# Kernel tuning notes

Measured on AMD Instinct MI355X. Metric: run time of the kernel, lower is better.

Reference implementation:

```python
import jax, jax.numpy as jnp
import numpy as np

NUM_USERS = 50000
EMBED_DIM = 128
NUM_EDGES = 800000


def setup_inputs() -> dict:
    key = jax.random.key(0)
    k1, k2, k3, k4, k5 = jax.random.split(key, 5)
    user_emb = jax.random.normal(k1, (NUM_USERS, EMBED_DIM), dtype=jnp.float32)
    # xavier_uniform init for the square weight
    limit = float(np.sqrt(6.0 / (EMBED_DIM + EMBED_DIM)))
    social_weight = jax.random.uniform(k2, (EMBED_DIM, EMBED_DIM), dtype=jnp.float32,
                                       minval=-limit, maxval=limit)
    rows = jax.random.randint(k3, (NUM_EDGES,), 0, NUM_USERS)  # destination nodes
    cols = jax.random.randint(k4, (NUM_EDGES,), 0, NUM_USERS)  # source nodes
    vals = jax.random.uniform(k5, (NUM_EDGES,), dtype=jnp.float32)  # adjacency weights
    return {"user_emb": user_emb, "social_weight": social_weight,
            "rows": rows, "cols": cols, "vals": vals}


def reference(user_emb, social_weight, rows, cols, vals):
    # weighted_emb = user_emb @ W  (dense GEMM)
    weighted = jnp.matmul(user_emb, social_weight)  # [N, D]
    # neighbor_emb = sparse.mm(adj, weighted): out[i] = sum_{e: rows[e]==i} vals[e] * weighted[cols[e]]
    gathered = weighted[cols] * vals[:, None]  # [E, D]
    neighbor = jax.ops.segment_sum(gathered, rows, num_segments=user_emb.shape[0])  # [N, D]
    # dropout is identity in eval mode; residual add
    return user_emb + neighbor
```

## Files before the change

### kernel.cpp

```cpp
#include <hip/hip_runtime.h>

#define DD 128
#define CAP 32
#define OVF_MAX 4096
#define EPB 2048
#define BSHIFT 10
#define NBKT_MAX 64
#define BCAP 24576

typedef __attribute__((ext_vector_type(8))) short short8;
typedef __attribute__((ext_vector_type(4))) float f32x4;

static __device__ __forceinline__ unsigned pack_bf16_2(float lo, float hi) {
  return __builtin_amdgcn_perm(__float_as_uint(hi) + 0x8000u,
                               __float_as_uint(lo) + 0x8000u, 0x07060302u);
}
static __device__ __forceinline__ unsigned short f2bf(float f) {
  return (unsigned short)((__float_as_uint(f) + 0x8000u) >> 16);
}
static __device__ __forceinline__ float bf2f(unsigned short h) {
  return __uint_as_float((unsigned)h << 16);
}

__global__ __launch_bounds__(256) void p1_bucket(
    const float* __restrict__ W, unsigned short* __restrict__ Wtg,
    const int* __restrict__ rows, const int* __restrict__ cols,
    const float* __restrict__ vals, int* __restrict__ binctr,
    int2* __restrict__ bucket, int* __restrict__ ovf_cnt,
    int4* __restrict__ ovf, int E, int nbkt) {
  const int t = threadIdx.x;
  if (blockIdx.x == 0) {
    const int k0 = (t >> 4) * 8;
    const int n0 = (t & 15) * 8;
    float v[8][8];
#pragma unroll
    for (int kk = 0; kk < 8; ++kk) {
      float4 a = *(const float4*)(W + (k0 + kk) * DD + n0);
      float4 b = *(const float4*)(W + (k0 + kk) * DD + n0 + 4);
      v[kk][0] = a.x; v[kk][1] = a.y; v[kk][2] = a.z; v[kk][3] = a.w;
      v[kk][4] = b.x; v[kk][5] = b.y; v[kk][6] = b.z; v[kk][7] = b.w;
    }
#pragma unroll
    for (int nn = 0; nn < 8; ++nn) {
      uint4 d;
      d.x = pack_bf16_2(v[0][nn], v[1][nn]);
      d.y = pack_bf16_2(v[2][nn], v[3][nn]);
      d.z = pack_bf16_2(v[4][nn], v[5][nn]);
      d.w = pack_bf16_2(v[6][nn], v[7][nn]);
      *(uint4*)(Wtg + (size_t)(n0 + nn) * DD + k0) = d;
    }
    return;
  }

  __shared__ int lrow[EPB];
  __shared__ int hist[NBKT_MAX];
  __shared__ int gbase[NBKT_MAX];
  __shared__ int lcur[NBKT_MAX];

  const int c0 = (blockIdx.x - 1) * EPB;
  const int n = min(EPB, E - c0);

  if (t < NBKT_MAX) { hist[t] = 0; lcur[t] = 0; }
  __syncthreads();

  for (int i = t; i < n; i += 256) {
    const int r = rows[c0 + i];
    lrow[i] = r;
    atomicAdd(&hist[r >> BSHIFT], 1);
  }
  __syncthreads();

  if (t < nbkt && hist[t] > 0) gbase[t] = atomicAdd(&binctr[t], hist[t]);
  __syncthreads();

  for (int i = t; i < n; i += 256) {
    const int r = lrow[i];
    const int b = r >> BSHIFT;
    const int lpos = atomicAdd(&lcur[b], 1);
    const int idx = gbase[b] + lpos;
    const int col = cols[c0 + i];
    const float v = vals[c0 + i];
    if (idx < BCAP) {
      bucket[(size_t)b * BCAP + idx] =
          make_int2(((r & 1023) << 22) | col, __float_as_int(v));
    } else {
      const int o = atomicAdd(ovf_cnt, 1);
      if (o < OVF_MAX) ovf[o] = make_int4(r, col, __float_as_int(v), 0);
    }
  }
}

#define WTS 136
__global__ __launch_bounds__(256) void p2k2_fused(
    const int* __restrict__ binctr, const int2* __restrict__ bucket,
    int* __restrict__ counts, int2* __restrict__ spair,
    int* __restrict__ ovf_cnt, int4* __restrict__ ovf,
    const float* __restrict__ U, const unsigned short* __restrict__ Wtg,
    unsigned short* __restrict__ wb, float* __restrict__ out, int N,
    int nbkt, int do_copy) {
  __shared__ union {
    unsigned short Wt[DD][WTS];
    int scnt[1 << BSHIFT];
  } sm;
  const int t = threadIdx.x;

  if ((int)blockIdx.x < nbkt) {
    const int b = blockIdx.x;
    const int base = b << BSHIFT;
    const int nrows = min(1 << BSHIFT, N - base);
    for (int i = t; i < (1 << BSHIFT); i += 256) sm.scnt[i] = 0;
    __syncthreads();

    const int nb = min(binctr[b], BCAP);
    const int2* __restrict__ bkt = bucket + (size_t)b * BCAP;
    for (int i = t; i < nb; i += 256) {
      const int2 p = bkt[i];
      const int lr = (unsigned)p.x >> 22;
      const int col = p.x & 0x3FFFFF;
      const int slot = atomicAdd(&sm.scnt[lr], 1);
      if (slot < CAP) {
        spair[(size_t)(base + lr) * CAP + slot] = make_int2(col, p.y);
      } else {
        const int o = atomicAdd(ovf_cnt, 1);
        if (o < OVF_MAX) ovf[o] = make_int4(base + lr, col, p.y, 0);
      }
    }
    __syncthreads();
    for (int i = t; i < nrows; i += 256) counts[base + i] = sm.scnt[i];
    return;
  }

  const int gb = blockIdx.x - nbkt;
#pragma unroll
  for (int i = 0; i < 8; ++i) {
    const int s = t + 256 * i;
    const int nn = s >> 4;
    const int k0 = (s & 15) * 8;
    uint4 d = *(const uint4*)(Wtg + (size_t)nn * DD + k0);
    *(uint4*)(&sm.Wt[nn][k0]) = d;
  }

  const int blk_row0 = gb * 128;
  if (do_copy) {
    const int nrow = min(128, N - blk_row0);
    const float4* U4 = (const float4*)(U + (size_t)blk_row0 * DD);
    float4* O4 = (float4*)(out + (size_t)blk_row0 * DD);
    for (int i = t; i < nrow * 32; i += 256) O4[i] = U4[i];
  }
  __syncthreads();

  const int w = t >> 6;
  const int lane = t & 63;
  const int m = lane & 15;
  const int quad = lane >> 4;
  const int row_base = blk_row0 + w * 32;

  short8 afrag[2][4];
#pragma unroll
  for (int s = 0; s < 2; ++s) {
    const int r = min(row_base + s * 16 + m, N - 1);
    const float* up = U + (size_t)r * DD + quad * 8;
#pragma unroll
    for (int c = 0; c < 4; ++c) {
      float4 x = *(const float4*)(up + c * 32);
      float4 y = *(const float4*)(up + c * 32 + 4);
      union { unsigned u[4]; short8 v; } fr;
      fr.u[0] = pack_bf16_2(x.x, x.y);
      fr.u[1] = pack_bf16_2(x.z, x.w);
      fr.u[2] = pack_bf16_2(y.x, y.y);
      fr.u[3] = pack_bf16_2(y.z, y.w);
      afrag[s][c] = fr.v;
    }
  }

  f32x4 acc[2][8];
#pragma unroll
  for (int s = 0; s < 2; ++s)
#pragma unroll
    for (int ct = 0; ct < 8; ++ct) acc[s][ct] = (f32x4){0.f, 0.f, 0.f, 0.f};

#pragma unroll
  for (int c = 0; c < 4; ++c) {
#pragma unroll
    for (int ct = 0; ct < 8; ++ct) {
      short8 bfrag = *(const short8*)&sm.Wt[ct * 16 + m][c * 32 + quad * 8];
      acc[0][ct] = __builtin_amdgcn_mfma_f32_16x16x32_bf16(
          afrag[0][c], bfrag, acc[0][ct], 0, 0, 0);
      acc[1][ct] = __builtin_amdgcn_mfma_f32_16x16x32_bf16(
          afrag[1][c], bfrag, acc[1][ct], 0, 0, 0);
    }
  }

#pragma unroll
  for (int s = 0; s < 2; ++s) {
    const int rb = row_base + s * 16 + quad * 4;
#pragma unroll
    for (int ct = 0; ct < 8; ++ct) {
#pragma unroll
      for (int reg = 0; reg < 4; ++reg) {
        const int r = rb + reg;
        if (r < N) wb[(size_t)r * DD + ct * 16 + m] = f2bf(acc[s][ct][reg]);
      }
    }
  }
}

__global__ __launch_bounds__(256) void k3_accumulate(
    const int* __restrict__ counts, const int2* __restrict__ spair,
    const unsigned short* __restrict__ wb, const float* __restrict__ U,
    const int* __restrict__ ovf_cnt, const int4* __restrict__ ovf,
    float* __restrict__ out, int N) {
  const int r = blockIdx.x * 4 + (threadIdx.x >> 6);
  if (r >= N) return;
  const int lane = threadIdx.x & 63;

  const ushort2* __restrict__ WB2 = (const ushort2*)wb;
  float2 acc = ((const float2*)U)[(size_t)r * 64 + lane];

  const int cnt = min(counts[r], CAP);
  const int2* __restrict__ lst = spair + (size_t)r * CAP;

  int i = 0;
  for (; i + 8 <= cnt; i += 8) {
    int2 p[8];
#pragma unroll
    for (int j = 0; j < 8; ++j) p[j] = lst[i + j];
    ushort2 a[8];
#pragma unroll
    for (int j = 0; j < 8; ++j) a[j] = WB2[(size_t)p[j].x * 64 + lane];
#pragma unroll
    for (int j = 0; j < 8; ++j) {
      const float v = __int_as_float(p[j].y);
      acc.x = fmaf(v, bf2f(a[j].x), acc.x);
      acc.y = fmaf(v, bf2f(a[j].y), acc.y);
    }
  }
  for (; i + 2 <= cnt; i += 2) {
    const int2 p0 = lst[i];
    const int2 p1 = lst[i + 1];
    const ushort2 a0 = WB2[(size_t)p0.x * 64 + lane];
    const ushort2 a1 = WB2[(size_t)p1.x * 64 + lane];
    const float v0 = __int_as_float(p0.y);
    const float v1 = __int_as_float(p1.y);
    acc.x = fmaf(v0, bf2f(a0.x), acc.x);
    acc.y = fmaf(v0, bf2f(a0.y), acc.y);
    acc.x = fmaf(v1, bf2f(a1.x), acc.x);
    acc.y = fmaf(v1, bf2f(a1.y), acc.y);
  }
  if (i < cnt) {
    const int2 p0 = lst[i];
    const ushort2 a0 = WB2[(size_t)p0.x * 64 + lane];
    const float v0 = __int_as_float(p0.y);
    acc.x = fmaf(v0, bf2f(a0.x), acc.x);
    acc.y = fmaf(v0, bf2f(a0.y), acc.y);
  }

  const int nov = min(*ovf_cnt, OVF_MAX);
  if (nov > 0) {
    for (int o = 0; o < nov; ++o) {
      const int4 e = ovf[o];
      if (e.x == r) {
        const float v = __int_as_float(e.z);
        const ushort2 a = WB2[(size_t)e.y * 64 + lane];
        acc.x = fmaf(v, bf2f(a.x), acc.x);
        acc.y = fmaf(v, bf2f(a.y), acc.y);
      }
    }
  }

  ((float2*)out)[(size_t)r * 64 + lane] = acc;
}

__global__ __launch_bounds__(256) void scatter_kernel(
    const int* __restrict__ rows, const int* __restrict__ cols,
    const float* __restrict__ vals, const unsigned short* __restrict__ wb,
    float* __restrict__ out, int E) {
  const int tid = blockIdx.x * 256 + threadIdx.x;
  const int e = tid >> 6;
  if (e >= E) return;
  const int lane = tid & 63;

  const int row = rows[e];
  const int col = cols[e];
  const float v = vals[e];

  const ushort2 w = ((const ushort2*)wb)[(size_t)col * 64 + lane];
  float* dst = out + (size_t)row * DD + lane * 2;
  unsafeAtomicAdd(dst, v * bf2f(w.x));
  unsafeAtomicAdd(dst + 1, v * bf2f(w.y));
}

static inline size_t align_up(size_t x, size_t a) { return (x + a - 1) & ~(a - 1); }

extern "C" void kernel_launch(void* const* d_in, const int* in_sizes, int n_in,
                              void* d_out, int out_size, void* d_ws, size_t ws_size,
                              hipStream_t stream) {
  const float* U = (const float*)d_in[0];
  const float* W = (const float*)d_in[1];
  const int* rows = (const int*)d_in[2];
  const int* cols = (const int*)d_in[3];
  const float* vals = (const float*)d_in[4];
  float* out = (float*)d_out;

  const int N = in_sizes[0] / DD;
  const int E = in_sizes[2];
  const int gemmBlocks = (N + 127) / 128;
  const int nchunks = (E + EPB - 1) / EPB;
  const int nbkt = (N + (1 << BSHIFT) - 1) >> BSHIFT;

  char* ws = (char*)d_ws;
  size_t off = 0;
  unsigned short* wb = (unsigned short*)(ws + off);
  off = align_up(off + (size_t)N * DD * sizeof(unsigned short), 16);
  unsigned short* Wtg = (unsigned short*)(ws + off);
  off = align_up(off + (size_t)DD * DD * sizeof(unsigned short), 16);
  int* counts = (int*)(ws + off);
  off = align_up(off + (size_t)N * sizeof(int), 16);
  int* binctr = (int*)(ws + off);
  int* ovf_cnt = binctr + NBKT_MAX;
  off = align_up(off + (NBKT_MAX + 4) * sizeof(int), 16);
  int4* ovf = (int4*)(ws + off);
  off = align_up(off + (size_t)OVF_MAX * sizeof(int4), 16);
  int2* bucket = (int2*)(ws + off);
  off = align_up(off + (size_t)nbkt * BCAP * sizeof(int2), 16);
  int2* spair = (int2*)(ws + off);
  off = align_up(off + (size_t)N * CAP * sizeof(int2), 16);
  const bool fast_ok = (off <= ws_size) && (nbkt <= NBKT_MAX);

  if (fast_ok) {
    hipMemsetAsync(binctr, 0, (NBKT_MAX + 1) * sizeof(int), stream);
    p1_bucket<<<1 + nchunks, 256, 0, stream>>>(
        W, Wtg, rows, cols, vals, binctr, bucket, ovf_cnt, ovf, E, nbkt);
    p2k2_fused<<<nbkt + gemmBlocks, 256, 0, stream>>>(
        binctr, bucket, counts, spair, ovf_cnt, ovf, U, Wtg, wb, out, N,
        nbkt, 0);
    k3_accumulate<<<(N + 3) / 4, 256, 0, stream>>>(
        counts, spair, wb, U, ovf_cnt, ovf, out, N);
  } else {
    p1_bucket<<<1, 256, 0, stream>>>(W, Wtg, rows, cols, vals, (int*)Wtg,
                                     (int2*)Wtg, (int*)Wtg, (int4*)Wtg, 0, 0);
    p2k2_fused<<<gemmBlocks, 256, 0, stream>>>(
        (const int*)Wtg, (const int2*)Wtg, (int*)Wtg, (int2*)Wtg, (int*)Wtg,
        (int4*)Wtg, U, Wtg, wb, out, N, 0, 1);
    const long long total = (long long)E * 64;
    scatter_kernel<<<(int)((total + 255) / 256), 256, 0, stream>>>(
        rows, cols, vals, wb, out, E);
  }
}
```

Measured before the change: 164.9 us.

## Fuse bucketing, GEMM and accumulation into one cooperative persistent kernel

Replaces three separate kernel launches (bucket, bucket-sort+GEMM, accumulate) with a single cooperative kernel that uses grid-wide syncs between phases. The grid is sized to nbkt+gemmBlocks (about 440 blocks), so the bucketing and accumulate phases loop over chunks and rows with that reduced block count. The W transpose is now redone in shared memory by every GEMM block instead of once into global memory, and the gather loop gains a 16-wide unroll. This removes launch gaps but limits parallelism in the memory-bound phases to the co-resident grid and adds grid-sync cost.

```diff
diff --git a/kernel.cpp b/kernel.cpp
--- a/kernel.cpp
+++ b/kernel.cpp
@@ -1,4 +1,7 @@
 #include <hip/hip_runtime.h>
+#include <hip/hip_cooperative_groups.h>
+
+namespace cg = cooperative_groups;
 
 #define DD 128
 #define CAP 32
@@ -7,6 +10,7 @@
 #define BSHIFT 10
 #define NBKT_MAX 64
 #define BCAP 24576
+#define WTS 136
 
 typedef __attribute__((ext_vector_type(8))) short short8;
 typedef __attribute__((ext_vector_type(4))) float f32x4;
@@ -20,6 +24,261 @@
 }
 static __device__ __forceinline__ float bf2f(unsigned short h) {
   return __uint_as_float((unsigned)h << 16);
+}
+
+__global__ __launch_bounds__(256, 2) void fused_all(
+    const float* __restrict__ U, const float* __restrict__ W,
+    const int* __restrict__ rows, const int* __restrict__ cols,
+    const float* __restrict__ vals, int* __restrict__ binctr,
+    int2* __restrict__ bucket, int* __restrict__ ovf_cnt,
+    int4* __restrict__ ovf, int* __restrict__ counts,
+    int2* __restrict__ spair, unsigned short* __restrict__ wb,
+    float* __restrict__ out, int N, int E, int nbkt) {
+  __shared__ union {
+    struct {
+      int lrow[EPB];
+      int hist[NBKT_MAX];
+      int gbase[NBKT_MAX];
+      int lcur[NBKT_MAX];
+    } p1;
+    unsigned short Wt[DD][WTS];
+    int scnt[1 << BSHIFT];
+  } sm;
+
+  const int t = threadIdx.x;
+  const int nblk = gridDim.x;
+
+  const int epb = max(1, min(EPB, (E + nblk - 1) / nblk));
+  const int nch = (E + epb - 1) / epb;
+  for (int ch = blockIdx.x; ch < nch; ch += nblk) {
+    const int c0 = ch * epb;
+    const int n = min(epb, E - c0);
+
+    if (t < NBKT_MAX) { sm.p1.hist[t] = 0; sm.p1.lcur[t] = 0; }
+    __syncthreads();
+
+    for (int i = t; i < n; i += 256) {
+      const int r = rows[c0 + i];
+      sm.p1.lrow[i] = r;
+      atomicAdd(&sm.p1.hist[r >> BSHIFT], 1);
+    }
+    __syncthreads();
+
+    if (t < nbkt && sm.p1.hist[t] > 0)
+      sm.p1.gbase[t] = atomicAdd(&binctr[t], sm.p1.hist[t]);
+    __syncthreads();
+
+    for (int i = t; i < n; i += 256) {
+      const int r = sm.p1.lrow[i];
+      const int b = r >> BSHIFT;
+      const int lpos = atomicAdd(&sm.p1.lcur[b], 1);
+      const int idx = sm.p1.gbase[b] + lpos;
+      const int col = cols[c0 + i];
+      const float v = vals[c0 + i];
+      if (idx < BCAP) {
+        bucket[(size_t)b * BCAP + idx] =
+            make_int2(((r & 1023) << 22) | col, __float_as_int(v));
+      } else {
+        const int o = atomicAdd(ovf_cnt, 1);
+        if (o < OVF_MAX) ovf[o] = make_int4(r, col, __float_as_int(v), 0);
+      }
+    }
+    __syncthreads();
+  }
+
+  __threadfence();
+  cg::this_grid().sync();
+
+  if ((int)blockIdx.x < nbkt) {
+    const int b = blockIdx.x;
+    const int base = b << BSHIFT;
+    const int nrows = min(1 << BSHIFT, N - base);
+    for (int i = t; i < (1 << BSHIFT); i += 256) sm.scnt[i] = 0;
+    __syncthreads();
+
+    const int nb = min(binctr[b], BCAP);
+    const int2* __restrict__ bkt = bucket + (size_t)b * BCAP;
+    for (int i = t; i < nb; i += 256) {
+      const int2 p = bkt[i];
+      const int lr = (unsigned)p.x >> 22;
+      const int col = p.x & 0x3FFFFF;
+      const int slot = atomicAdd(&sm.scnt[lr], 1);
+      if (slot < CAP) {
+        spair[(size_t)(base + lr) * CAP + slot] = make_int2(col, p.y);
+      } else {
+        const int o = atomicAdd(ovf_cnt, 1);
+        if (o < OVF_MAX) ovf[o] = make_int4(base + lr, col, p.y, 0);
+      }
+    }
+    __syncthreads();
+    for (int i = t; i < nrows; i += 256) counts[base + i] = sm.scnt[i];
+  } else {
+    const int gb = blockIdx.x - nbkt;
+    const int gemmBlocks = (N + 127) >> 7;
+    if (gb < gemmBlocks) {
+      {
+        const int k0 = (t >> 4) * 8;
+        const int n0 = (t & 15) * 8;
+        float v[8][8];
+#pragma unroll
+        for (int kk = 0; kk < 8; ++kk) {
+          float4 a = *(const float4*)(W + (k0 + kk) * DD + n0);
+          float4 b = *(const float4*)(W + (k0 + kk) * DD + n0 + 4);
+          v[kk][0] = a.x; v[kk][1] = a.y; v[kk][2] = a.z; v[kk][3] = a.w;
+          v[kk][4] = b.x; v[kk][5] = b.y; v[kk][6] = b.z; v[kk][7] = b.w;
+        }
+#pragma unroll
+        for (int nn = 0; nn < 8; ++nn) {
+          uint4 d;
+          d.x = pack_bf16_2(v[0][nn], v[1][nn]);
+          d.y = pack_bf16_2(v[2][nn], v[3][nn]);
+          d.z = pack_bf16_2(v[4][nn], v[5][nn]);
+          d.w = pack_bf16_2(v[6][nn], v[7][nn]);
+          *(uint4*)(&sm.Wt[n0 + nn][k0]) = d;
+        }
+      }
+      __syncthreads();
+
+      const int blk_row0 = gb * 128;
+      const int w = t >> 6;
+      const int lane = t & 63;
+      const int m = lane & 15;
+      const int quad = lane >> 4;
+      const int row_base = blk_row0 + w * 32;
+
+      short8 afrag[2][4];
+#pragma unroll
+      for (int s = 0; s < 2; ++s) {
+        const int r = min(row_base + s * 16 + m, N - 1);
+        const float* up = U + (size_t)r * DD + quad * 8;
+#pragma unroll
+        for (int c = 0; c < 4; ++c) {
+          float4 x = *(const float4*)(up + c * 32);
+          float4 y = *(const float4*)(up + c * 32 + 4);
+          union { unsigned u[4]; short8 v; } fr;
+          fr.u[0] = pack_bf16_2(x.x, x.y);
+          fr.u[1] = pack_bf16_2(x.z, x.w);
+          fr.u[2] = pack_bf16_2(y.x, y.y);
+          fr.u[3] = pack_bf16_2(y.z, y.w);
+          afrag[s][c] = fr.v;
+        }
+      }
+
+      f32x4 acc[2][8];
+#pragma unroll
+      for (int s = 0; s < 2; ++s)
+#pragma unroll
+        for (int ct = 0; ct < 8; ++ct) acc[s][ct] = (f32x4){0.f, 0.f, 0.f, 0.f};
+
+#pragma unroll
+      for (int c = 0; c < 4; ++c) {
+#pragma unroll
+        for (int ct = 0; ct < 8; ++ct) {
+          short8 bfrag = *(const short8*)&sm.Wt[ct * 16 + m][c * 32 + quad * 8];
+          acc[0][ct] = __builtin_amdgcn_mfma_f32_16x16x32_bf16(
+              afrag[0][c], bfrag, acc[0][ct], 0, 0, 0);
+          acc[1][ct] = __builtin_amdgcn_mfma_f32_16x16x32_bf16(
+              afrag[1][c], bfrag, acc[1][ct], 0, 0, 0);
+        }
+      }
+
+#pragma unroll
+      for (int s = 0; s < 2; ++s) {
+        const int rb = row_base + s * 16 + quad * 4;
+#pragma unroll
+        for (int ct = 0; ct < 8; ++ct) {
+#pragma unroll
+          for (int reg = 0; reg < 4; ++reg) {
+            const int r = rb + reg;
+            if (r < N) wb[(size_t)r * DD + ct * 16 + m] = f2bf(acc[s][ct][reg]);
+          }
+        }
+      }
+    }
+  }
+
+  __threadfence();
+  cg::this_grid().sync();
+
+  {
+    const int lane = t & 63;
+    const int wsel = t >> 6;
+    const ushort2* __restrict__ WB2 = (const ushort2*)wb;
+    const int ntask = (N + 3) >> 2;
+    const int nov = min(*ovf_cnt, OVF_MAX);
+
+    for (int task = blockIdx.x; task < ntask; task += nblk) {
+      const int r = task * 4 + wsel;
+      if (r >= N) continue;
+
+      float2 acc = ((const float2*)U)[(size_t)r * 64 + lane];
+      const int cnt = min(counts[r], CAP);
+      const int2* __restrict__ lst = spair + (size_t)r * CAP;
+
+      int i = 0;
+      for (; i + 16 <= cnt; i += 16) {
+        int2 p[16];
+#pragma unroll
+        for (int j = 0; j < 16; ++j) p[j] = lst[i + j];
+        ushort2 a[16];
+#pragma unroll
+        for (int j = 0; j < 16; ++j) a[j] = WB2[(size_t)p[j].x * 64 + lane];
+#pragma unroll
+        for (int j = 0; j < 16; ++j) {
+          const float v = __int_as_float(p[j].y);
+          acc.x = fmaf(v, bf2f(a[j].x), acc.x);
+          acc.y = fmaf(v, bf2f(a[j].y), acc.y);
+        }
+      }
+      for (; i + 8 <= cnt; i += 8) {
+        int2 p[8];
+#pragma unroll
+        for (int j = 0; j < 8; ++j) p[j] = lst[i + j];
+        ushort2 a[8];
+#pragma unroll
+        for (int j = 0; j < 8; ++j) a[j] = WB2[(size_t)p[j].x * 64 + lane];
+#pragma unroll
+        for (int j = 0; j < 8; ++j) {
+          const float v = __int_as_float(p[j].y);
+          acc.x = fmaf(v, bf2f(a[j].x), acc.x);
+          acc.y = fmaf(v, bf2f(a[j].y), acc.y);
+        }
+      }
+      for (; i + 2 <= cnt; i += 2) {
+        const int2 p0 = lst[i];
+        const int2 p1 = lst[i + 1];
+        const ushort2 a0 = WB2[(size_t)p0.x * 64 + lane];
+        const ushort2 a1 = WB2[(size_t)p1.x * 64 + lane];
+        const float v0 = __int_as_float(p0.y);
+        const float v1 = __int_as_float(p1.y);
+        acc.x = fmaf(v0, bf2f(a0.x), acc.x);
+        acc.y = fmaf(v0, bf2f(a0.y), acc.y);
+        acc.x = fmaf(v1, bf2f(a1.x), acc.x);
+        acc.y = fmaf(v1, bf2f(a1.y), acc.y);
+      }
+      if (i < cnt) {
+        const int2 p0 = lst[i];
+        const ushort2 a0 = WB2[(size_t)p0.x * 64 + lane];
+        const float v0 = __int_as_float(p0.y);
+        acc.x = fmaf(v0, bf2f(a0.x), acc.x);
+        acc.y = fmaf(v0, bf2f(a0.y), acc.y);
+      }
+
+      if (nov > 0) {
+        for (int o = 0; o < nov; ++o) {
+          const int4 e = ovf[o];
+          if (e.x == r) {
+            const float v = __int_as_float(e.z);
+            const ushort2 a = WB2[(size_t)e.y * 64 + lane];
+            acc.x = fmaf(v, bf2f(a.x), acc.x);
+            acc.y = fmaf(v, bf2f(a.y), acc.y);
+          }
+        }
+      }
+
+      ((float2*)out)[(size_t)r * 64 + lane] = acc;
+    }
+  }
 }
 
 __global__ __launch_bounds__(256) void p1_bucket(
@@ -51,28 +310,22 @@
     }
     return;
   }
-
   __shared__ int lrow[EPB];
   __shared__ int hist[NBKT_MAX];
   __shared__ int gbase[NBKT_MAX];
   __shared__ int lcur[NBKT_MAX];
-
   const int c0 = (blockIdx.x - 1) * EPB;
   const int n = min(EPB, E - c0);
-
   if (t < NBKT_MAX) { hist[t] = 0; lcur[t] = 0; }
   __syncthreads();
-
   for (int i = t; i < n; i += 256) {
     const int r = rows[c0 + i];
     lrow[i] = r;
     atomicAdd(&hist[r >> BSHIFT], 1);
   }
   __syncthreads();
-
   if (t < nbkt && hist[t] > 0) gbase[t] = atomicAdd(&binctr[t], hist[t]);
   __syncthreads();
-
   for (int i = t; i < n; i += 256) {
     const int r = lrow[i];
     const int b = r >> BSHIFT;
@@ -90,7 +343,6 @@
   }
 }
 
-#define WTS 136
 __global__ __launch_bounds__(256) void p2k2_fused(
     const int* __restrict__ binctr, const int2* __restrict__ bucket,
     int* __restrict__ counts, int2* __restrict__ spair,
@@ -110,7 +362,6 @@
     const int nrows = min(1 << BSHIFT, N - base);
     for (int i = t; i < (1 << BSHIFT); i += 256) sm.scnt[i] = 0;
     __syncthreads();
-
     const int nb = min(binctr[b], BCAP);
     const int2* __restrict__ bkt = bucket + (size_t)b * BCAP;
     for (int i = t; i < nb; i += 256) {
@@ -205,72 +456,6 @@
   }
 }
 
-__global__ __launch_bounds__(256) void k3_accumulate(
-    const int* __restrict__ counts, const int2* __restrict__ spair,
-    const unsigned short* __restrict__ wb, const float* __restrict__ U,
-    const int* __restrict__ ovf_cnt, const int4* __restrict__ ovf,
-    float* __restrict__ out, int N) {
-  const int r = blockIdx.x * 4 + (threadIdx.x >> 6);
-  if (r >= N) return;
-  const int lane = threadIdx.x & 63;
-
-  const ushort2* __restrict__ WB2 = (const ushort2*)wb;
-  float2 acc = ((const float2*)U)[(size_t)r * 64 + lane];
-
-  const int cnt = min(counts[r], CAP);
-  const int2* __restrict__ lst = spair + (size_t)r * CAP;
-
-  int i = 0;
-  for (; i + 8 <= cnt; i += 8) {
-    int2 p[8];
-#pragma unroll
-    for (int j = 0; j < 8; ++j) p[j] = lst[i + j];
-    ushort2 a[8];
-#pragma unroll
-    for (int j = 0; j < 8; ++j) a[j] = WB2[(size_t)p[j].x * 64 + lane];
-#pragma unroll
-    for (int j = 0; j < 8; ++j) {
-      const float v = __int_as_float(p[j].y);
-      acc.x = fmaf(v, bf2f(a[j].x), acc.x);
-      acc.y = fmaf(v, bf2f(a[j].y), acc.y);
-    }
-  }
-  for (; i + 2 <= cnt; i += 2) {
-    const int2 p0 = lst[i];
-    const int2 p1 = lst[i + 1];
-    const ushort2 a0 = WB2[(size_t)p0.x * 64 + lane];
-    const ushort2 a1 = WB2[(size_t)p1.x * 64 + lane];
-    const float v0 = __int_as_float(p0.y);
-    const float v1 = __int_as_float(p1.y);
-    acc.x = fmaf(v0, bf2f(a0.x), acc.x);
-    acc.y = fmaf(v0, bf2f(a0.y), acc.y);
-    acc.x = fmaf(v1, bf2f(a1.x), acc.x);
-    acc.y = fmaf(v1, bf2f(a1.y), acc.y);
-  }
-  if (i < cnt) {
-    const int2 p0 = lst[i];
-    const ushort2 a0 = WB2[(size_t)p0.x * 64 + lane];
-    const float v0 = __int_as_float(p0.y);
-    acc.x = fmaf(v0, bf2f(a0.x), acc.x);
-    acc.y = fmaf(v0, bf2f(a0.y), acc.y);
-  }
-
-  const int nov = min(*ovf_cnt, OVF_MAX);
-  if (nov > 0) {
-    for (int o = 0; o < nov; ++o) {
-      const int4 e = ovf[o];
-      if (e.x == r) {
-        const float v = __int_as_float(e.z);
-        const ushort2 a = WB2[(size_t)e.y * 64 + lane];
-        acc.x = fmaf(v, bf2f(a.x), acc.x);
-        acc.y = fmaf(v, bf2f(a.y), acc.y);
-      }
-    }
-  }
-
-  ((float2*)out)[(size_t)r * 64 + lane] = acc;
-}
-
 __global__ __launch_bounds__(256) void scatter_kernel(
     const int* __restrict__ rows, const int* __restrict__ cols,
     const float* __restrict__ vals, const unsigned short* __restrict__ wb,
@@ -305,8 +490,8 @@
   const int N = in_sizes[0] / DD;
   const int E = in_sizes[2];
   const int gemmBlocks = (N + 127) / 128;
-  const int nchunks = (E + EPB - 1) / EPB;
   const int nbkt = (N + (1 << BSHIFT) - 1) >> BSHIFT;
+  const int grid = nbkt + gemmBlocks;
 
   char* ws = (char*)d_ws;
   size_t off = 0;
@@ -325,17 +510,20 @@
   off = align_up(off + (size_t)nbkt * BCAP * sizeof(int2), 16);
   int2* spair = (int2*)(ws + off);
   off = align_up(off + (size_t)N * CAP * sizeof(int2), 16);
-  const bool fast_ok = (off <= ws_size) && (nbkt <= NBKT_MAX);
+  const bool fast_ok =
+      (off <= ws_size) && (nbkt <= NBKT_MAX) && (grid <= 512) && (E > 0);
 
   if (fast_ok) {
     hipMemsetAsync(binctr, 0, (NBKT_MAX + 1) * sizeof(int), stream);
-    p1_bucket<<<1 + nchunks, 256, 0, stream>>>(
-        W, Wtg, rows, cols, vals, binctr, bucket, ovf_cnt, ovf, E, nbkt);
-    p2k2_fused<<<nbkt + gemmBlocks, 256, 0, stream>>>(
-        binctr, bucket, counts, spair, ovf_cnt, ovf, U, Wtg, wb, out, N,
-        nbkt, 0);
-    k3_accumulate<<<(N + 3) / 4, 256, 0, stream>>>(
-        counts, spair, wb, U, ovf_cnt, ovf, out, N);
+    int N_ = N, E_ = E, nbkt_ = nbkt;
+    void* args[] = {(void*)&U,      (void*)&W,      (void*)&rows,
+                    (void*)&cols,   (void*)&vals,   (void*)&binctr,
+                    (void*)&bucket, (void*)&ovf_cnt,(void*)&ovf,
+                    (void*)&counts, (void*)&spair,  (void*)&wb,
+                    (void*)&out,    (void*)&N_,     (void*)&E_,
+                    (void*)&nbkt_};
+    hipLaunchCooperativeKernel((const void*)fused_all, dim3(grid), dim3(256),
+                               args, 0, stream);
   } else {
     p1_bucket<<<1, 256, 0, stream>>>(W, Wtg, rows, cols, vals, (int*)Wtg,
                                      (int2*)Wtg, (int*)Wtg, (int4*)Wtg, 0, 0);
```

Measured after the change: 440.9 us. 167% more time.
